# Optimization experiments

Hardware: AMD Instinct MI355X
Metric: run time of the kernel (lower is better)

## Reference

```python
import jax, jax.numpy as jnp
import numpy as np

D_MODEL = 1024
NUM_HEADS = 16
D_K = D_MODEL // NUM_HEADS


def setup_inputs() -> dict:
    key = jax.random.key(0)
    ks = jax.random.split(key, 11)
    B, S, D = 2, 2048, D_MODEL
    s = 1.0 / np.sqrt(D)
    return {
        "Q": jax.random.normal(ks[0], (B, S, D), jnp.float32),
        "K": jax.random.normal(ks[1], (B, S, D), jnp.float32),
        "V": jax.random.normal(ks[2], (B, S, D), jnp.float32),
        "Wq": jax.random.normal(ks[3], (D, D), jnp.float32) * s,
        "bq": jax.random.normal(ks[4], (D,), jnp.float32) * s,
        "Wk": jax.random.normal(ks[5], (D, D), jnp.float32) * s,
        "bk": jax.random.normal(ks[6], (D,), jnp.float32) * s,
        "Wv": jax.random.normal(ks[7], (D, D), jnp.float32) * s,
        "bv": jax.random.normal(ks[8], (D,), jnp.float32) * s,
        "Wo": jax.random.normal(ks[9], (D, D), jnp.float32) * s,
        "bo": jax.random.normal(ks[10], (D,), jnp.float32) * s,
    }


def _split_heads(x):
    B, S, D = x.shape
    return x.reshape(B, S, NUM_HEADS, D_K).transpose(0, 2, 1, 3)  # [B,H,S,d_k]


def reference(Q, K, V, Wq, bq, Wk, bk, Wv, bv, Wo, bo):
    q = _split_heads(Q @ Wq + bq)
    k = _split_heads(K @ Wk + bk)
    v = _split_heads(V @ Wv + bv)
    scale = 1.0 / np.sqrt(D_K)
    scores = jnp.einsum('bhqd,bhkd->bhqk', q, k) * scale
    P = jax.nn.softmax(scores, axis=-1)  # max-subtract + exp + normalize
    O = jnp.einsum('bhqk,bhkd->bhqd', P, v)
    B, H, S, dk = O.shape
    O = O.transpose(0, 2, 1, 3).reshape(B, S, H * dk)
    return O @ Wo + bo
```

## Files before the change

### kernel.cpp

```cpp
#include <hip/hip_runtime.h>
#include <math.h>

#define S_LEN 2048
#define DMODEL 1024
#define NHEADS 16
#define DK 64

#define QSCALE 0.1803368801111244f

typedef __attribute__((ext_vector_type(8))) _Float16 f16x8;
typedef __attribute__((ext_vector_type(2))) __fp16 hf16x2;
typedef __attribute__((ext_vector_type(4))) float f32x4;

static __device__ __forceinline__ unsigned short f2h(float f) {
    _Float16 h = (_Float16)f;
    return __builtin_bit_cast(unsigned short, h);
}

static __device__ __forceinline__ unsigned pack2(float a, float b) {
    hf16x2 h = __builtin_amdgcn_cvt_pkrtz(a, b);
    return __builtin_bit_cast(unsigned, h);
}

static __device__ __forceinline__ void gload16(const void* g, void* l) {
    __builtin_amdgcn_global_load_lds(
        (const __attribute__((address_space(1))) void*)g,
        (__attribute__((address_space(3))) void*)l, 16, 0, 0);
}

__global__ __launch_bounds__(256)
void cvt_f16_kernel(const float* __restrict__ s0, const float* __restrict__ s1,
                    const float* __restrict__ s2, unsigned short* __restrict__ d)
{
    const int z = blockIdx.y;
    const float* src = z == 0 ? s0 : (z == 1 ? s1 : s2);
    unsigned short* dst = d + (size_t)z * 4194304;
    const int i = (blockIdx.x * 256 + threadIdx.x) * 8;
    float4 a = *reinterpret_cast<const float4*>(src + i);
    float4 b = *reinterpret_cast<const float4*>(src + i + 4);
    uint4 o;
    o.x = (unsigned)f2h(a.x) | ((unsigned)f2h(a.y) << 16);
    o.y = (unsigned)f2h(a.z) | ((unsigned)f2h(a.w) << 16);
    o.z = (unsigned)f2h(b.x) | ((unsigned)f2h(b.y) << 16);
    o.w = (unsigned)f2h(b.z) | ((unsigned)f2h(b.w) << 16);
    *reinterpret_cast<uint4*>(dst + i) = o;
}

__global__ __launch_bounds__(256)
void wprep_kernel(const float* __restrict__ w0, const float* __restrict__ w1,
                  const float* __restrict__ w2, const float* __restrict__ w3,
                  unsigned short* __restrict__ wt)
{
    __shared__ float tile[64][65];
    const int z = blockIdx.z;
    const float* W = z == 0 ? w0 : (z == 1 ? w1 : (z == 2 ? w2 : w3));
    unsigned short* Wt = wt + (size_t)z * 1048576;
    const int k0 = blockIdx.x * 64, n0 = blockIdx.y * 64;
    const int t = threadIdx.x;
    #pragma unroll
    for (int i = 0; i < 4; ++i) {
        int idx = i * 256 + t;
        int r = idx >> 4, c4 = (idx & 15) * 4;
        float4 v = *reinterpret_cast<const float4*>(W + (size_t)(k0 + r) * 1024 + n0 + c4);
        tile[r][c4 + 0] = v.x; tile[r][c4 + 1] = v.y;
        tile[r][c4 + 2] = v.z; tile[r][c4 + 3] = v.w;
    }
    __syncthreads();
    #pragma unroll
    for (int i = 0; i < 4; ++i) {
        int idx = i * 256 + t;
        int nr = idx >> 4, kc4 = (idx & 15) * 4;
        ushort4 h;
        h.x = f2h(tile[kc4 + 0][nr]); h.y = f2h(tile[kc4 + 1][nr]);
        h.z = f2h(tile[kc4 + 2][nr]); h.w = f2h(tile[kc4 + 3][nr]);
        *reinterpret_cast<ushort4*>(Wt + (size_t)(n0 + nr) * 1024 + k0 + kc4) = h;
    }
}

__global__ __launch_bounds__(256)
void gemm_mfma_kernel(const unsigned short* __restrict__ xh_base,
                      const unsigned short* __restrict__ wt_base,
                      const float* __restrict__ b0, const float* __restrict__ b1,
                      const float* __restrict__ b2,
                      void* __restrict__ dst_base, int mode_base)
{
    __shared__ short Als[128 * 64];
    __shared__ short Bls[64 * 64];

    const int z = blockIdx.z;
    const unsigned short* Ag = xh_base + (size_t)z * 4194304;
    const unsigned short* Bg = wt_base + (size_t)z * 1048576;
    const float* bias = z == 0 ? b0 : (z == 1 ? b1 : b2);
    const int mode = mode_base < 0 ? z : mode_base;

    const int tid = threadIdx.x;
    const int w = tid >> 6, l = tid & 63, a = l & 15, g = l >> 4;
    const int wm = w >> 1, wn = w & 1;
    const int bm = blockIdx.x * 128, bn = blockIdx.y * 64;

    f32x4 acc[4][2] = {};

    for (int k0 = 0; k0 < 1024; k0 += 64) {
        #pragma unroll
        for (int r2 = 0; r2 < 4; ++r2) {
            int idx = r2 * 256 + tid;
            gload16(Ag + (size_t)(bm + (idx >> 3)) * 1024 + k0 + (idx & 7) * 8,
                    (char*)Als + (size_t)(r2 * 256 + w * 64) * 16);
        }
        #pragma unroll
        for (int r2 = 0; r2 < 2; ++r2) {
            int idx = r2 * 256 + tid;
            gload16(Bg + (size_t)(bn + (idx >> 3)) * 1024 + k0 + (idx & 7) * 8,
                    (char*)Bls + (size_t)(r2 * 256 + w * 64) * 16);
        }
        __syncthreads();
        #pragma unroll
        for (int kc = 0; kc < 2; ++kc) {
            f16x8 af[4], bf[2];
            #pragma unroll
            for (int mi = 0; mi < 4; ++mi)
                af[mi] = *reinterpret_cast<const f16x8*>(
                    &Als[(wm * 64 + 16 * mi + a) * 64 + kc * 32 + g * 8]);
            #pragma unroll
            for (int ni = 0; ni < 2; ++ni)
                bf[ni] = *reinterpret_cast<const f16x8*>(
                    &Bls[(wn * 32 + 16 * ni + a) * 64 + kc * 32 + g * 8]);
            #pragma unroll
            for (int mi = 0; mi < 4; ++mi)
                #pragma unroll
                for (int ni = 0; ni < 2; ++ni)
                    acc[mi][ni] = __builtin_amdgcn_mfma_f32_16x16x32_f16(
                        af[mi], bf[ni], acc[mi][ni], 0, 0, 0);
        }
        __syncthreads();
    }

    void* mydst = (mode == 3) ? dst_base
                 : (void*)((unsigned short*)dst_base + (size_t)z * 4194304);

    #pragma unroll
    for (int ni = 0; ni < 2; ++ni) {
        const int n = bn + wn * 32 + 16 * ni + a;
        const float bv = bias[n];
        #pragma unroll
        for (int mi = 0; mi < 4; ++mi) {
            const int mbase = bm + wm * 64 + 16 * mi + g * 4;
            if (mode == 3) {
                float* o = (float*)mydst;
                #pragma unroll
                for (int r = 0; r < 4; ++r)
                    o[(size_t)(mbase + r) * 1024 + n] = acc[mi][ni][r] + bv;
            } else if (mode == 2) {
                unsigned short* o = (unsigned short*)mydst;
                const int b = mbase >> 11, s = mbase & (S_LEN - 1);
                const int h = n >> 6, d = n & (DK - 1);
                ushort4 st;
                st.x = f2h(acc[mi][ni][0] + bv);
                st.y = f2h(acc[mi][ni][1] + bv);
                st.z = f2h(acc[mi][ni][2] + bv);
                st.w = f2h(acc[mi][ni][3] + bv);
                *reinterpret_cast<ushort4*>(
                    o + ((size_t)((b * NHEADS + h) * DK + d)) * S_LEN + s) = st;
            } else {
                unsigned short* o = (unsigned short*)mydst;
                const float sc = (mode == 0) ? QSCALE : 1.0f;
                #pragma unroll
                for (int r = 0; r < 4; ++r) {
                    const int m = mbase + r;
                    const int b = m >> 11, s = m & (S_LEN - 1);
                    const int h = n >> 6, d = n & (DK - 1);
                    o[((size_t)((b * NHEADS + h) * S_LEN + s)) * DK + d] =
                        f2h((acc[mi][ni][r] + bv) * sc);
                }
            }
        }
    }
}

__global__ __launch_bounds__(512, 4)
void attn_mfma_kernel(const unsigned short* __restrict__ qb,
                      const unsigned short* __restrict__ kb,
                      const unsigned short* __restrict__ vt,
                      unsigned short* __restrict__ ob)
{
    __shared__ char Kls[2][8192];
    __shared__ char Vls[2][8192];
    __shared__ unsigned short Pl[8][32][72];

    const int tid = threadIdx.x;
    const int w = tid >> 6;
    const int p = w >> 2;
    const int wsub = w & 3;
    const int l = tid & 63;
    const int a = l & 15;
    const int g = l >> 4;
    const int bh = blockIdx.y;
    const int q0 = blockIdx.x * 128 + wsub * 32;

    const unsigned short* qhead = qb + (size_t)bh * S_LEN * DK;
    const char* khead = (const char*)(kb + (size_t)bh * S_LEN * DK);
    const char* vhead = (const char*)(vt + (size_t)bh * DK * S_LEN);

    f16x8 qf[2][2];
    #pragma unroll
    for (int j = 0; j < 2; ++j)
        #pragma unroll
        for (int c = 0; c < 2; ++c)
            qf[j][c] = *reinterpret_cast<const f16x8*>(
                qhead + (size_t)(q0 + 16 * j + a) * DK + 32 * c + 8 * g);

    f16x8 onesf;
    #pragma unroll
    for (int i = 0; i < 8; ++i) onesf[i] = (_Float16)1.f;

    f32x4 oacc[4][2] = {};
    f32x4 lacc[2] = {};
    float mrun[2] = {-INFINITY, -INFINITY};

    const int srow = tid >> 3;
    const int sgc = ((tid & 7) << 4) ^ ((srow & 7) << 4);

    #define STAGE1(t2)                                                          \
        do {                                                                    \
            gload16(khead + (size_t)((t2) * 64 + srow) * 128 + sgc,             \
                    &Kls[(t2) & 1][(size_t)w * 1024]);                          \
            gload16(vhead + (size_t)srow * 4096 + (size_t)(t2) * 128 + sgc,     \
                    &Vls[(t2) & 1][(size_t)w * 1024]);                          \
        } while (0)

    STAGE1(0);
    STAGE1(1);
    __syncthreads();

    for (int i = 0; i < 16; ++i) {
        f16x8 kf[2][4];
        #pragma unroll
        for (int c = 0; c < 2; ++c)
            #pragma unroll
            for (int T = 0; T < 4; ++T) {
                const int row = 16 * T + a;
                kf[c][T] = *reinterpret_cast<const f16x8*>(
                    &Kls[p][row * 128 + ((64 * c + 16 * g) ^ ((row & 7) << 4))]);
            }

        #pragma unroll
        for (int j = 0; j < 2; ++j) {
            f32x4 sacc[4] = {};
            __builtin_amdgcn_s_setprio(1);
            #pragma unroll
            for (int c = 0; c < 2; ++c)
                #pragma unroll
                for (int T = 0; T < 4; ++T)
                    sacc[T] = __builtin_amdgcn_mfma_f32_16x16x32_f16(
                        kf[c][T], qf[j][c], sacc[T], 0, 0, 0);
            __builtin_amdgcn_s_setprio(0);

            float lm = -INFINITY;
            #pragma unroll
            for (int T = 0; T < 4; ++T)
                #pragma unroll
                for (int r = 0; r < 4; ++r) lm = fmaxf(lm, sacc[T][r]);

            if (!__all(lm <= mrun[j] + 8.f)) {
                float vmax = fmaxf(lm, __shfl_xor(lm, 16));
                vmax = fmaxf(vmax, __shfl_xor(vmax, 32));
                const float mnew = fmaxf(mrun[j], vmax);
                const float corr = __builtin_amdgcn_exp2f(mrun[j] - mnew);
                #pragma unroll
                for (int t = 0; t < 4; ++t) {
                    oacc[t][j][0] *= corr; oacc[t][j][1] *= corr;
                    oacc[t][j][2] *= corr; oacc[t][j][3] *= corr;
                }
                lacc[j][0] *= corr; lacc[j][1] *= corr;
                lacc[j][2] *= corr; lacc[j][3] *= corr;
                mrun[j] = mnew;
            }

            const float mj = mrun[j];
            #pragma unroll
            for (int T = 0; T < 4; ++T) {
                float e0 = __builtin_amdgcn_exp2f(sacc[T][0] - mj);
                float e1 = __builtin_amdgcn_exp2f(sacc[T][1] - mj);
                float e2 = __builtin_amdgcn_exp2f(sacc[T][2] - mj);
                float e3 = __builtin_amdgcn_exp2f(sacc[T][3] - mj);
                unsigned* dst = reinterpret_cast<unsigned*>(
                    &Pl[w][16 * j + a][16 * T + 4 * g]);
                dst[0] = pack2(e0, e1);
                dst[1] = pack2(e2, e3);
            }
        }

        f16x8 vf[2][4];
        #pragma unroll
        for (int c = 0; c < 2; ++c)
            #pragma unroll
            for (int t = 0; t < 4; ++t) {
                const int row = 16 * t + a;
                vf[c][t] = *reinterpret_cast<const f16x8*>(
                    &Vls[p][row * 128 + ((64 * c + 16 * g) ^ ((row & 7) << 4))]);
            }

        __syncthreads();
        if (i < 15) {
            STAGE1(2 * i + 2);
            STAGE1(2 * i + 3);
        }

        #pragma unroll
        for (int c = 0; c < 2; ++c) {
            f16x8 pf[2];
            #pragma unroll
            for (int j = 0; j < 2; ++j)
                pf[j] = *reinterpret_cast<const f16x8*>(
                    &Pl[w][16 * j + a][32 * c + 8 * g]);
            __builtin_amdgcn_s_setprio(1);
            #pragma unroll
            for (int t = 0; t < 4; ++t)
                #pragma unroll
                for (int j = 0; j < 2; ++j)
                    oacc[t][j] = __builtin_amdgcn_mfma_f32_16x16x32_f16(
                        vf[c][t], pf[j], oacc[t][j], 0, 0, 0);
            #pragma unroll
            for (int j = 0; j < 2; ++j)
                lacc[j] = __builtin_amdgcn_mfma_f32_16x16x32_f16(
                    onesf, pf[j], lacc[j], 0, 0, 0);
            __builtin_amdgcn_s_setprio(0);
        }
        __syncthreads();
    }
    #undef STAGE1

    float* Ob = (float*)Pl;
    float* Ml = (float*)Kls;
    if (p == 1) {
        #pragma unroll
        for (int j = 0; j < 2; ++j) {
            if (g == 0) {
                Ml[((wsub * 2 + j) * 2 + 0) * 16 + a] = mrun[j];
                Ml[((wsub * 2 + j) * 2 + 1) * 16 + a] = lacc[j][0];
            }
            #pragma unroll
            for (int t = 0; t < 4; ++t)
                #pragma unroll
                for (int r = 0; r < 4; ++r)
                    Ob[((wsub * 2 + j) * 64 + 16 * t + 4 * g + r) * 16 + a] =
                        oacc[t][j][r];
        }
    }
    __syncthreads();
    if (p == 0) {
        const int b = bh >> 4;
        const int h = bh & (NHEADS - 1);
        #pragma unroll
        for (int j = 0; j < 2; ++j) {
            const float m1 = Ml[((wsub * 2 + j) * 2 + 0) * 16 + a];
            const float l1 = Ml[((wsub * 2 + j) * 2 + 1) * 16 + a];
            const float m0 = mrun[j];
            const float ms = fmaxf(m0, m1);
            const float c0 = __builtin_amdgcn_exp2f(m0 - ms);
            const float c1 = __builtin_amdgcn_exp2f(m1 - ms);
            const float inv = 1.f / (lacc[j][0] * c0 + l1 * c1);
            unsigned short* dst0 =
                ob + (size_t)(b * S_LEN + q0 + 16 * j + a) * DMODEL + h * DK;
            #pragma unroll
            for (int t = 0; t < 4; ++t) {
                ushort4 st;
                #pragma unroll
                for (int r = 0; r < 4; ++r) {
                    const float o1 =
                        Ob[((wsub * 2 + j) * 64 + 16 * t + 4 * g + r) * 16 + a];
                    const float val = (oacc[t][j][r] * c0 + o1 * c1) * inv;
                    ((unsigned short*)&st)[r] = f2h(val);
                }
                *reinterpret_cast<ushort4*>(dst0 + 16 * t + 4 * g) = st;
            }
        }
    }
}

extern "C" void kernel_launch(void* const* d_in, const int* in_sizes, int n_in,
                              void* d_out, int out_size, void* d_ws, size_t ws_size,
                              hipStream_t stream)
{
    const float* Q  = (const float*)d_in[0];
    const float* K  = (const float*)d_in[1];
    const float* V  = (const float*)d_in[2];
    const float* Wq = (const float*)d_in[3];
    const float* bq = (const float*)d_in[4];
    const float* Wk = (const float*)d_in[5];
    const float* bk = (const float*)d_in[6];
    const float* Wv = (const float*)d_in[7];
    const float* bv = (const float*)d_in[8];
    const float* Wo = (const float*)d_in[9];
    const float* bo = (const float*)d_in[10];
    float* out = (float*)d_out;

    unsigned short* xh  = (unsigned short*)d_ws;
    unsigned short* wt  = xh + (size_t)3 * 4194304;
    unsigned short* qb  = wt + (size_t)4 * 1048576;
    unsigned short* kb  = qb + 4194304;
    unsigned short* vtb = kb + 4194304;
    unsigned short* obh = vtb + 4194304;

    cvt_f16_kernel<<<dim3(2048, 3), 256, 0, stream>>>(Q, K, V, xh);
    wprep_kernel<<<dim3(16, 16, 4), 256, 0, stream>>>(Wq, Wk, Wv, Wo, wt);

    gemm_mfma_kernel<<<dim3(32, 16, 3), 256, 0, stream>>>(
        xh, wt, bq, bk, bv, qb, -1);

    attn_mfma_kernel<<<dim3(S_LEN / 128, 2 * NHEADS), 512, 0, stream>>>(qb, kb, vtb, obh);

    gemm_mfma_kernel<<<dim3(32, 16, 1), 256, 0, stream>>>(
        obh, wt + (size_t)3 * 1048576, bo, bo, bo, out, 3);
}
```

Baseline: 137.2 us.

## Enlarge projection GEMM tiles to 128x128 with swizzled LDS and MFMA priority

Reworks the projection GEMM to use 128x128 output tiles with 512 threads (8 waves), doubling per-block reuse of the staged A and B tiles and halving global loads per output. LDS rows are XOR-swizzled in 16-byte chunks to reduce bank conflicts on the fragment reads, and wave priority is raised around the MFMA block. The input conversion kernel switches to the packed round-toward-zero convert. Fewer blocks may reduce occupancy or tail balance, and RTZ rounding slightly changes numerics.

```diff
diff --git a/kernel.cpp b/kernel.cpp
--- a/kernel.cpp
+++ b/kernel.cpp
@@ -39,10 +39,10 @@
     float4 a = *reinterpret_cast<const float4*>(src + i);
     float4 b = *reinterpret_cast<const float4*>(src + i + 4);
     uint4 o;
-    o.x = (unsigned)f2h(a.x) | ((unsigned)f2h(a.y) << 16);
-    o.y = (unsigned)f2h(a.z) | ((unsigned)f2h(a.w) << 16);
-    o.z = (unsigned)f2h(b.x) | ((unsigned)f2h(b.y) << 16);
-    o.w = (unsigned)f2h(b.z) | ((unsigned)f2h(b.w) << 16);
+    o.x = pack2(a.x, a.y);
+    o.y = pack2(a.z, a.w);
+    o.z = pack2(b.x, b.y);
+    o.w = pack2(b.z, b.w);
     *reinterpret_cast<uint4*>(dst + i) = o;
 }
 
@@ -77,60 +77,66 @@
     }
 }
 
-__global__ __launch_bounds__(256)
+__global__ __launch_bounds__(512)
 void gemm_mfma_kernel(const unsigned short* __restrict__ xh_base,
                       const unsigned short* __restrict__ wt_base,
                       const float* __restrict__ b0, const float* __restrict__ b1,
                       const float* __restrict__ b2,
                       void* __restrict__ dst_base, int mode_base)
 {
-    __shared__ short Als[128 * 64];
-    __shared__ short Bls[64 * 64];
+    __shared__ char Als[16384];
+    __shared__ char Bls[16384];
 
     const int z = blockIdx.z;
-    const unsigned short* Ag = xh_base + (size_t)z * 4194304;
-    const unsigned short* Bg = wt_base + (size_t)z * 1048576;
+    const char* Ag = (const char*)(xh_base + (size_t)z * 4194304);
+    const char* Bg = (const char*)(wt_base + (size_t)z * 1048576);
     const float* bias = z == 0 ? b0 : (z == 1 ? b1 : b2);
     const int mode = mode_base < 0 ? z : mode_base;
 
     const int tid = threadIdx.x;
     const int w = tid >> 6, l = tid & 63, a = l & 15, g = l >> 4;
-    const int wm = w >> 1, wn = w & 1;
-    const int bm = blockIdx.x * 128, bn = blockIdx.y * 64;
+    const int wm = w >> 2, wn = w & 3;
+    const int bm = blockIdx.y * 128, bn = blockIdx.x * 128;
+
+    const int srow = tid >> 3;
+    const int sc8 = tid & 7;
 
     f32x4 acc[4][2] = {};
 
-    for (int k0 = 0; k0 < 1024; k0 += 64) {
-        #pragma unroll
-        for (int r2 = 0; r2 < 4; ++r2) {
-            int idx = r2 * 256 + tid;
-            gload16(Ag + (size_t)(bm + (idx >> 3)) * 1024 + k0 + (idx & 7) * 8,
-                    (char*)Als + (size_t)(r2 * 256 + w * 64) * 16);
-        }
-        #pragma unroll
-        for (int r2 = 0; r2 < 2; ++r2) {
-            int idx = r2 * 256 + tid;
-            gload16(Bg + (size_t)(bn + (idx >> 3)) * 1024 + k0 + (idx & 7) * 8,
-                    (char*)Bls + (size_t)(r2 * 256 + w * 64) * 16);
+    for (int k0b = 0; k0b < 2048; k0b += 128) {
+        #pragma unroll
+        for (int it = 0; it < 2; ++it) {
+            const int row = it * 64 + srow;
+            const int gc = (sc8 << 4) ^ ((row & 7) << 4);
+            gload16(Ag + (size_t)(bm + row) * 2048 + k0b + gc,
+                    &Als[(size_t)(it * 512 + tid) * 16]);
+            gload16(Bg + (size_t)(bn + row) * 2048 + k0b + gc,
+                    &Bls[(size_t)(it * 512 + tid) * 16]);
         }
         __syncthreads();
         #pragma unroll
         for (int kc = 0; kc < 2; ++kc) {
             f16x8 af[4], bf[2];
             #pragma unroll
-            for (int mi = 0; mi < 4; ++mi)
+            for (int mi = 0; mi < 4; ++mi) {
+                const int row = wm * 64 + 16 * mi + a;
                 af[mi] = *reinterpret_cast<const f16x8*>(
-                    &Als[(wm * 64 + 16 * mi + a) * 64 + kc * 32 + g * 8]);
-            #pragma unroll
-            for (int ni = 0; ni < 2; ++ni)
+                    &Als[row * 128 + ((kc * 64 + g * 16) ^ ((row & 7) << 4))]);
+            }
+            #pragma unroll
+            for (int ni = 0; ni < 2; ++ni) {
+                const int row = wn * 32 + 16 * ni + a;
                 bf[ni] = *reinterpret_cast<const f16x8*>(
-                    &Bls[(wn * 32 + 16 * ni + a) * 64 + kc * 32 + g * 8]);
+                    &Bls[row * 128 + ((kc * 64 + g * 16) ^ ((row & 7) << 4))]);
+            }
+            __builtin_amdgcn_s_setprio(1);
             #pragma unroll
             for (int mi = 0; mi < 4; ++mi)
                 #pragma unroll
                 for (int ni = 0; ni < 2; ++ni)
                     acc[mi][ni] = __builtin_amdgcn_mfma_f32_16x16x32_f16(
                         af[mi], bf[ni], acc[mi][ni], 0, 0, 0);
+            __builtin_amdgcn_s_setprio(0);
         }
         __syncthreads();
     }
@@ -405,11 +411,11 @@
     cvt_f16_kernel<<<dim3(2048, 3), 256, 0, stream>>>(Q, K, V, xh);
     wprep_kernel<<<dim3(16, 16, 4), 256, 0, stream>>>(Wq, Wk, Wv, Wo, wt);
 
-    gemm_mfma_kernel<<<dim3(32, 16, 3), 256, 0, stream>>>(
+    gemm_mfma_kernel<<<dim3(8, 32, 3), 512, 0, stream>>>(
         xh, wt, bq, bk, bv, qb, -1);
 
     attn_mfma_kernel<<<dim3(S_LEN / 128, 2 * NHEADS), 512, 0, stream>>>(qb, kb, vtb, obh);
 
-    gemm_mfma_kernel<<<dim3(32, 16, 1), 256, 0, stream>>>(
+    gemm_mfma_kernel<<<dim3(8, 32, 1), 512, 0, stream>>>(
         obh, wt + (size_t)3 * 1048576, bo, bo, bo, out, 3);
 }
```

Measured after the change: 137.1 us. About the same (-0.0%).
